# Kernel tuning notes

Measured on AMD Instinct MI355X. Metric: run time of the kernel, lower is better.

## Reference

```python
import jax, jax.numpy as jnp
import numpy as np

EMBED = 1024
DSTATE = 16
DCONV = 4
DTRANK = 64  # ceil(EMBED/16)
B = 2
T = 2048


def setup_inputs() -> dict:
    key = jax.random.key(0)
    ks = jax.random.split(key, 8)
    def w(k, shape, s=0.02):
        return jax.random.normal(k, shape, dtype=jnp.float32) * s
    return dict(
        x=jax.random.normal(ks[0], (B, T, EMBED), dtype=jnp.float32),
        in_proj_w=w(ks[1], (2 * EMBED, EMBED)), in_proj_b=jnp.zeros((2 * EMBED,), jnp.float32),
        conv_w=w(ks[2], (EMBED, 1, DCONV)), conv_b=jnp.zeros((EMBED,), jnp.float32),
        x_proj_w=w(ks[3], (DTRANK + 2 * DSTATE, EMBED)), x_proj_b=jnp.zeros((DTRANK + 2 * DSTATE,), jnp.float32),
        dt_proj_w=w(ks[4], (EMBED, DTRANK)), dt_proj_b=jnp.zeros((EMBED,), jnp.float32),
        A_log=jnp.log(jnp.arange(1, DSTATE + 1, dtype=jnp.float32))[None, :],  # (1,N) as in torch module
        D_param=jnp.ones((EMBED,), jnp.float32),
        out_proj_w=w(ks[5], (EMBED, EMBED)), out_proj_b=jnp.zeros((EMBED,), jnp.float32),
        skip_proj_w=w(ks[6], (EMBED, EMBED)), skip_proj_b=jnp.zeros((EMBED,), jnp.float32),
    )


def reference(x, in_proj_w, in_proj_b, conv_w, conv_b, x_proj_w, x_proj_b,
              dt_proj_w, dt_proj_b, A_log, D_param, out_proj_w, out_proj_b,
              skip_proj_w, skip_proj_b):
    Bsz, Tlen, Dm = x.shape
    # in_proj and split into ssm branch and gate branch
    xr = x @ in_proj_w.T + in_proj_b            # (B,T,2D)
    x_in, res = jnp.split(xr, 2, axis=-1)
    # depthwise causal conv1d (torch pads both sides then slices [:T] == left-pad)
    xc = jax.lax.conv_general_dilated(
        x_in.transpose(0, 2, 1), conv_w, (1,), [(DCONV - 1, 0)],
        dimension_numbers=('NCH', 'OIH', 'NCH'), feature_group_count=Dm)
    xc = (xc + conv_b[None, :, None]).transpose(0, 2, 1)  # (B,T,D)
    xc = jax.nn.silu(xc)
    # input-dependent SSM params
    ssm = xc @ x_proj_w.T + x_proj_b            # (B,T,dt_rank+2N)
    delta, Bp, Cp = jnp.split(ssm, [DTRANK, DTRANK + DSTATE], axis=-1)
    delta = jax.nn.softplus(delta @ dt_proj_w.T + dt_proj_b)  # (B,T,D)
    A = -jnp.exp(A_log)                          # (1,N)
    dA = jnp.exp(delta[..., None] * A)           # (B,T,D,N)
    dBu = delta[..., None] * Bp[:, :, None, :] * xc[..., None]  # (B,T,D,N)
    # inclusive associative scan over time: h_t = dA_t * h_{t-1} + dBu_t
    def op(l, r):
        Ai, Bi = l
        Aj, Bj = r
        return (Aj * Ai, Bj + Aj * Bi)
    _, ys = jax.lax.associative_scan(op, (dA, dBu), axis=1)
    y = (ys * Cp[:, :, None, :]).sum(-1)         # (B,T,D)
    y = y + xc * D_param
    y = y * jax.nn.silu(res)
    return y @ out_proj_w.T + out_proj_b + (x @ skip_proj_w.T + skip_proj_b)
```

## Files before the change

### kernel.cpp

```cpp
#include <hip/hip_runtime.h>
#include <math.h>

#define EMBED  1024
#define DSTATE 16
#define DCONV  4
#define DTRANK 64
#define BB     2
#define TT     2048
#define M_TOK  (BB*TT)
#define SSMW   96
#define NCHUNK 64
#define CLEN   (TT/NCHUNK)
#define KSPLIT 8

typedef __attribute__((ext_vector_type(8))) __bf16 bf16x8;
typedef __attribute__((ext_vector_type(4))) float floatx4;

__device__ __forceinline__ float silu_f(float x) {
    return x / (1.0f + __expf(-x));
}
__device__ __forceinline__ float softplus_f(float x) {
    return fmaxf(x, 0.0f) + log1pf(__expf(-fabsf(x)));
}
__device__ __forceinline__ unsigned short f2bf(float f) {
    union { float f; unsigned int u; } v; v.f = f;
    unsigned int u = v.u;
    return (unsigned short)((u + 0x7fffu + ((u >> 16) & 1u)) >> 16);
}
__device__ __forceinline__ float bf2f(unsigned short s) {
    union { unsigned int u; float f; } v; v.u = ((unsigned int)s) << 16;
    return v.f;
}
__device__ __forceinline__ void async16(unsigned short* lds, const unsigned short* g) {
    __builtin_amdgcn_global_load_lds(
        (const __attribute__((address_space(1))) unsigned int*)g,
        (__attribute__((address_space(3))) unsigned int*)lds, 16, 0, 0);
}

#define GEMM_DECODE \
    const int tid = threadIdx.x; const int wid = tid >> 6; \
    const int lane = tid & 63; \
    const int wm = wid >> 1, wn = wid & 1; \
    const int lr = lane & 15; const int lq = lane >> 4;

__device__ __forceinline__ void gemm_acc(
    const unsigned short* __restrict__ A, int lda,
    const unsigned short* __restrict__ W, int ldw,
    int m0, int n0, int k0, int klen, floatx4 (&acc)[4][4])
{
    __shared__ unsigned short As[128 * 32];
    __shared__ unsigned short Ws[128 * 32];
    GEMM_DECODE;
    const int l0 = tid,       row0 = l0 >> 2, kc0 = (l0 & 3) * 8;
    const int l1 = tid + 256, row1 = l1 >> 2, kc1 = (l1 & 3) * 8;

    for (int kt = k0; kt < k0 + klen; kt += 32) {
        async16(&As[l0 * 8], A + (size_t)(m0 + row0) * lda + kt + kc0);
        async16(&As[l1 * 8], A + (size_t)(m0 + row1) * lda + kt + kc1);
        async16(&Ws[l0 * 8], W + (size_t)(n0 + row0) * ldw + kt + kc0);
        async16(&Ws[l1 * 8], W + (size_t)(n0 + row1) * ldw + kt + kc1);
        __syncthreads();

        bf16x8 af[4], bfr[4];
        #pragma unroll
        for (int i = 0; i < 4; ++i)
            af[i] = *(const bf16x8*)&As[(wm * 64 + i * 16 + lr) * 32 + lq * 8];
        #pragma unroll
        for (int i = 0; i < 4; ++i)
            bfr[i] = *(const bf16x8*)&Ws[(wn * 64 + i * 16 + lr) * 32 + lq * 8];

        #pragma unroll
        for (int mi = 0; mi < 4; ++mi)
            #pragma unroll
            for (int ni = 0; ni < 4; ++ni)
                acc[mi][ni] = __builtin_amdgcn_mfma_f32_16x16x32_bf16(
                    af[mi], bfr[ni], acc[mi][ni], 0, 0, 0);
        __syncthreads();
    }
}

__global__ __launch_bounds__(256)
void gemm_in(const unsigned short* __restrict__ A,
             const unsigned short* __restrict__ W,
             const float* __restrict__ bias,
             float* __restrict__ xr, unsigned short* __restrict__ gate)
{
    floatx4 acc[4][4] = {};
    const int m0 = blockIdx.x * 128, n0 = blockIdx.y * 128;
    gemm_acc(A, 2 * EMBED, W, EMBED, m0, n0, 0, EMBED, acc);
    GEMM_DECODE;
    #pragma unroll
    for (int mi = 0; mi < 4; ++mi)
        #pragma unroll
        for (int ni = 0; ni < 4; ++ni) {
            int nb = n0 + wn * 64 + ni * 16 + lr;
            #pragma unroll
            for (int r = 0; r < 4; ++r) {
                int m = m0 + wm * 64 + mi * 16 + lq * 4 + r;
                float v = acc[mi][ni][r] + bias[nb];
                if (nb < EMBED) xr[(size_t)m * EMBED + nb] = v;
                else gate[(size_t)m * EMBED + nb - EMBED] = f2bf(silu_f(v));
            }
        }
}

__global__ __launch_bounds__(256)
void gemm_xp(const unsigned short* __restrict__ A,
             const unsigned short* __restrict__ W,
             float* __restrict__ xpart)
{
    floatx4 acc[4][4] = {};
    const int m0 = blockIdx.x * 128;
    const int k0 = blockIdx.z * (EMBED / KSPLIT);
    gemm_acc(A, EMBED, W, EMBED, m0, 0, k0, EMBED / KSPLIT, acc);
    GEMM_DECODE;
    float* base = xpart + (size_t)blockIdx.z * M_TOK * SSMW;
    #pragma unroll
    for (int mi = 0; mi < 4; ++mi)
        #pragma unroll
        for (int ni = 0; ni < 4; ++ni) {
            int nb = wn * 64 + ni * 16 + lr;
            if (nb < SSMW) {
                #pragma unroll
                for (int r = 0; r < 4; ++r) {
                    int m = m0 + wm * 64 + mi * 16 + lq * 4 + r;
                    base[(size_t)m * SSMW + nb] = acc[mi][ni][r];
                }
            }
        }
}

__global__ __launch_bounds__(256)
void xp_merge(const float* __restrict__ xpart, const float* __restrict__ xp_b,
              float* __restrict__ ssm, unsigned short* __restrict__ dtin)
{
    int idx = blockIdx.x * 256 + threadIdx.x;
    if (idx >= M_TOK * SSMW) return;
    int m = idx / SSMW, n = idx - m * SSMW;
    float s = xp_b[n];
    #pragma unroll
    for (int z = 0; z < KSPLIT; ++z) s += xpart[(size_t)z * M_TOK * SSMW + idx];
    ssm[idx] = s;
    if (n < DTRANK) dtin[(size_t)m * DTRANK + n] = f2bf(s);
}

__global__ __launch_bounds__(256)
void gemm_dt(const unsigned short* __restrict__ A,
             const unsigned short* __restrict__ W,
             const float* __restrict__ bias,
             unsigned short* __restrict__ dltb)
{
    floatx4 acc[4][4] = {};
    const int m0 = blockIdx.x * 128, n0 = blockIdx.y * 128;
    gemm_acc(A, DTRANK, W, DTRANK, m0, n0, 0, DTRANK, acc);
    GEMM_DECODE;
    #pragma unroll
    for (int mi = 0; mi < 4; ++mi)
        #pragma unroll
        for (int ni = 0; ni < 4; ++ni) {
            int nb = n0 + wn * 64 + ni * 16 + lr;
            #pragma unroll
            for (int r = 0; r < 4; ++r) {
                int m = m0 + wm * 64 + mi * 16 + lq * 4 + r;
                dltb[(size_t)m * EMBED + nb] = f2bf(softplus_f(acc[mi][ni][r] + bias[nb]));
            }
        }
}

__global__ __launch_bounds__(256)
void gemm_out(const unsigned short* __restrict__ A,
              const unsigned short* __restrict__ W,
              const float* __restrict__ bias, const float* __restrict__ bias2,
              float* __restrict__ C)
{
    floatx4 acc[4][4] = {};
    const int m0 = blockIdx.x * 128, n0 = blockIdx.y * 128;
    gemm_acc(A, 2 * EMBED, W, 2 * EMBED, m0, n0, 0, 2 * EMBED, acc);
    GEMM_DECODE;
    #pragma unroll
    for (int mi = 0; mi < 4; ++mi)
        #pragma unroll
        for (int ni = 0; ni < 4; ++ni) {
            int nb = n0 + wn * 64 + ni * 16 + lr;
            float bb = bias[nb] + bias2[nb];
            #pragma unroll
            for (int r = 0; r < 4; ++r) {
                int m = m0 + wm * 64 + mi * 16 + lq * 4 + r;
                C[(size_t)m * EMBED + nb] = acc[mi][ni][r] + bb;
            }
        }
}

#define SEG0 524288
#define SEG1 (SEG0 + 16384)
#define SEG2 (SEG1 + 32768)
#define SEG3 (SEG2 + 524288)
#define SEG4 (SEG3 + 1048576)

__global__ __launch_bounds__(256)
void cvt_pack(const float* __restrict__ in_w, const float* __restrict__ dt_w,
              const float* __restrict__ xp_w, const float* __restrict__ ow,
              const float* __restrict__ sw, const float* __restrict__ x,
              unsigned short* __restrict__ inwb, unsigned short* __restrict__ dtwb,
              unsigned short* __restrict__ xpwb, unsigned short* __restrict__ wcat,
              unsigned short* __restrict__ Acat)
{
    int j = blockIdx.x * 256 + threadIdx.x;
    if (j >= SEG4) return;
    float4 v = {0.f, 0.f, 0.f, 0.f};
    unsigned short* dst;
    if (j < SEG0) {
        v = *(const float4*)&in_w[j * 4];
        dst = &inwb[j * 4];
    } else if (j < SEG1) {
        int i = (j - SEG0) * 4;
        v = *(const float4*)&dt_w[i];
        dst = &dtwb[i];
    } else if (j < SEG2) {
        int i = (j - SEG1) * 4;
        if ((i >> 10) < SSMW) v = *(const float4*)&xp_w[i];
        dst = &xpwb[i];
    } else if (j < SEG3) {
        int i = (j - SEG2) * 4;
        int n = i >> 11, k = i & 2047;
        v = *(const float4*)((k < EMBED) ? &ow[(size_t)n * EMBED + k]
                                         : &sw[(size_t)n * EMBED + (k - EMBED)]);
        dst = &wcat[i];
    } else {
        int i = (j - SEG3) * 4;
        int m = i >> 10, k = i & 1023;
        v = *(const float4*)&x[i];
        dst = &Acat[(size_t)m * 2 * EMBED + EMBED + k];
    }
    ushort4 o = { f2bf(v.x), f2bf(v.y), f2bf(v.z), f2bf(v.w) };
    *(ushort4*)dst = o;
}

__global__ __launch_bounds__(256)
void conv_silu(const float* __restrict__ xr,
               const float* __restrict__ conv_w,
               const float* __restrict__ conv_b,
               unsigned short* __restrict__ xcb)
{
    int idx = blockIdx.x * 256 + threadIdx.x;
    if (idx >= BB * TT * EMBED / 4) return;
    int dq = idx & (EMBED / 4 - 1);
    int t  = (idx >> 8) & (TT - 1);
    int b  = idx >> 19;
    int d  = dq * 4;

    float4 cw0 = *(const float4*)&conv_w[(d + 0) * 4];
    float4 cw1 = *(const float4*)&conv_w[(d + 1) * 4];
    float4 cw2 = *(const float4*)&conv_w[(d + 2) * 4];
    float4 cw3 = *(const float4*)&conv_w[(d + 3) * 4];
    float4 s   = *(const float4*)&conv_b[d];

    const float* w0 = (const float*)&cw0;
    const float* w1 = (const float*)&cw1;
    const float* w2 = (const float*)&cw2;
    const float* w3 = (const float*)&cw3;

    #pragma unroll
    for (int jj = 0; jj < 4; ++jj) {
        int tr = t - 3 + jj;
        if (tr >= 0) {
            float4 v = *(const float4*)&xr[(size_t)(b * TT + tr) * EMBED + d];
            s.x = fmaf(w0[jj], v.x, s.x);
            s.y = fmaf(w1[jj], v.y, s.y);
            s.z = fmaf(w2[jj], v.z, s.z);
            s.w = fmaf(w3[jj], v.w, s.w);
        }
    }
    ushort4 o = { f2bf(silu_f(s.x)), f2bf(silu_f(s.y)),
                  f2bf(silu_f(s.z)), f2bf(silu_f(s.w)) };
    *(ushort4*)&xcb[(size_t)(b * TT + t) * EMBED + d] = o;
}

__global__ __launch_bounds__(256)
void scan_chunk(const unsigned short* __restrict__ deltab,
                const unsigned short* __restrict__ xcb,
                const float* __restrict__ ssm,
                const float* __restrict__ A_log,
                float* __restrict__ hout,
                float* __restrict__ Ssum)
{
    __shared__ float Bs[CLEN][DSTATE];
    const int tid = threadIdx.x;
    const int blk = blockIdx.x;
    const int dg = blk & 3, chunk = (blk >> 2) & (NCHUNK - 1), b = blk >> 8;
    const int d = dg * 256 + tid;
    const int t0 = chunk * CLEN;

    for (int i = tid; i < CLEN * DSTATE; i += 256) {
        int t = i >> 4, n = i & 15;
        Bs[t][n] = ssm[(size_t)(b * TT + t0 + t) * SSMW + DTRANK + n];
    }
    __syncthreads();

    float An[DSTATE];
    #pragma unroll
    for (int n = 0; n < DSTATE; ++n) An[n] = -__expf(A_log[n]);

    float h[DSTATE] = {};
    float S = 0.f;
    for (int t = 0; t < CLEN; ++t) {
        size_t row = (size_t)(b * TT + t0 + t);
        float dv = bf2f(deltab[row * EMBED + d]);
        float xv = bf2f(xcb[row * EMBED + d]);
        S += dv;
        float sx = dv * xv;
        float Bv[DSTATE];
        *(float4*)&Bv[0]  = *(const float4*)&Bs[t][0];
        *(float4*)&Bv[4]  = *(const float4*)&Bs[t][4];
        *(float4*)&Bv[8]  = *(const float4*)&Bs[t][8];
        *(float4*)&Bv[12] = *(const float4*)&Bs[t][12];
        #pragma unroll
        for (int n = 0; n < DSTATE; ++n) {
            float dA = __expf(dv * An[n]);
            h[n] = fmaf(dA, h[n], sx * Bv[n]);
        }
    }
    size_t base = ((size_t)(chunk * BB + b) * EMBED + d) * DSTATE;
    #pragma unroll
    for (int jj = 0; jj < 4; ++jj)
        *(float4*)&hout[base + jj * 4] = *(float4*)&h[jj * 4];
    Ssum[(size_t)(chunk * BB + b) * EMBED + d] = S;
}

__global__ __launch_bounds__(256)
void scan_combine(const float* __restrict__ A_log,
                  const float* __restrict__ Ssum,
                  const float* __restrict__ hout,
                  float* __restrict__ hin)
{
    int idx = blockIdx.x * 256 + threadIdx.x;
    int n  = idx & 15;
    int bd = idx >> 4;
    float An = -__expf(A_log[n]);
    float h = 0.f;
    for (int c0 = 0; c0 < NCHUNK; c0 += 8) {
        float ho[8], S[8];
        #pragma unroll
        for (int jj = 0; jj < 8; ++jj) {
            ho[jj] = hout[(size_t)(c0 + jj) * (BB * EMBED * DSTATE) + idx];
            S[jj]  = Ssum[(size_t)(c0 + jj) * (BB * EMBED) + bd];
        }
        #pragma unroll
        for (int jj = 0; jj < 8; ++jj) {
            hin[(size_t)(c0 + jj) * (BB * EMBED * DSTATE) + idx] = h;
            h = fmaf(__expf(An * S[jj]), h, ho[jj]);
        }
    }
}

__global__ __launch_bounds__(256)
void scan_apply(const unsigned short* __restrict__ deltab,
                const unsigned short* __restrict__ xcb,
                const float* __restrict__ ssm,
                const float* __restrict__ A_log,
                const float* __restrict__ D_param,
                const unsigned short* __restrict__ gate,
                const float* __restrict__ hin,
                unsigned short* __restrict__ Acat)
{
    __shared__ float Bs[CLEN][DSTATE];
    __shared__ float Cs[CLEN][DSTATE];
    const int tid = threadIdx.x;
    const int blk = blockIdx.x;
    const int dg = blk & 3, chunk = (blk >> 2) & (NCHUNK - 1), b = blk >> 8;
    const int d = dg * 256 + tid;
    const int t0 = chunk * CLEN;

    for (int i = tid; i < CLEN * DSTATE; i += 256) {
        int t = i >> 4, n = i & 15;
        size_t row = (size_t)(b * TT + t0 + t);
        Bs[t][n] = ssm[row * SSMW + DTRANK + n];
        Cs[t][n] = ssm[row * SSMW + DTRANK + DSTATE + n];
    }
    __syncthreads();

    float An[DSTATE];
    #pragma unroll
    for (int n = 0; n < DSTATE; ++n) An[n] = -__expf(A_log[n]);
    float Dd = D_param[d];

    float h[DSTATE];
    size_t base = ((size_t)(chunk * BB + b) * EMBED + d) * DSTATE;
    #pragma unroll
    for (int jj = 0; jj < 4; ++jj)
        *(float4*)&h[jj * 4] = *(const float4*)&hin[base + jj * 4];

    for (int t = 0; t < CLEN; ++t) {
        size_t row = (size_t)(b * TT + t0 + t);
        float dv = bf2f(deltab[row * EMBED + d]);
        float xv = bf2f(xcb[row * EMBED + d]);
        float sx = dv * xv;
        float Bv[DSTATE], Cv[DSTATE];
        *(float4*)&Bv[0]  = *(const float4*)&Bs[t][0];
        *(float4*)&Bv[4]  = *(const float4*)&Bs[t][4];
        *(float4*)&Bv[8]  = *(const float4*)&Bs[t][8];
        *(float4*)&Bv[12] = *(const float4*)&Bs[t][12];
        *(float4*)&Cv[0]  = *(const float4*)&Cs[t][0];
        *(float4*)&Cv[4]  = *(const float4*)&Cs[t][4];
        *(float4*)&Cv[8]  = *(const float4*)&Cs[t][8];
        *(float4*)&Cv[12] = *(const float4*)&Cs[t][12];
        float y0 = 0.f, y1 = 0.f, y2 = 0.f, y3 = 0.f;
        #pragma unroll
        for (int n = 0; n < DSTATE; n += 4) {
            float dA0 = __expf(dv * An[n + 0]);
            float dA1 = __expf(dv * An[n + 1]);
            float dA2 = __expf(dv * An[n + 2]);
            float dA3 = __expf(dv * An[n + 3]);
            h[n + 0] = fmaf(dA0, h[n + 0], sx * Bv[n + 0]);
            h[n + 1] = fmaf(dA1, h[n + 1], sx * Bv[n + 1]);
            h[n + 2] = fmaf(dA2, h[n + 2], sx * Bv[n + 2]);
            h[n + 3] = fmaf(dA3, h[n + 3], sx * Bv[n + 3]);
            y0 = fmaf(h[n + 0], Cv[n + 0], y0);
            y1 = fmaf(h[n + 1], Cv[n + 1], y1);
            y2 = fmaf(h[n + 2], Cv[n + 2], y2);
            y3 = fmaf(h[n + 3], Cv[n + 3], y3);
        }
        float yv = (y0 + y1) + (y2 + y3) + xv * Dd;
        float g = bf2f(gate[row * EMBED + d]);
        Acat[row * 2 * EMBED + d] = f2bf(yv * g);
    }
}

extern "C" void kernel_launch(void* const* d_in, const int* in_sizes, int n_in,
                              void* d_out, int out_size, void* d_ws, size_t ws_size,
                              hipStream_t stream) {
    const float* x      = (const float*)d_in[0];
    const float* in_w   = (const float*)d_in[1];
    const float* in_b   = (const float*)d_in[2];
    const float* conv_w = (const float*)d_in[3];
    const float* conv_b = (const float*)d_in[4];
    const float* xp_w   = (const float*)d_in[5];
    const float* xp_b   = (const float*)d_in[6];
    const float* dt_w   = (const float*)d_in[7];
    const float* dt_b   = (const float*)d_in[8];
    const float* A_log  = (const float*)d_in[9];
    const float* Dp     = (const float*)d_in[10];
    const float* out_w  = (const float*)d_in[11];
    const float* out_b  = (const float*)d_in[12];
    const float* skip_w = (const float*)d_in[13];
    const float* skip_b = (const float*)d_in[14];
    float* out = (float*)d_out;

    float* ws    = (float*)d_ws;
    float* xr    = ws;
    float* ssm   = xr    + (size_t)M_TOK * EMBED;
    float* xpart = ssm   + (size_t)M_TOK * SSMW;
    float* hout  = xpart + (size_t)KSPLIT * M_TOK * SSMW;
    float* hin   = hout  + (size_t)NCHUNK * BB * EMBED * DSTATE;
    float* Ssum  = hin   + (size_t)NCHUNK * BB * EMBED * DSTATE;
    unsigned short* Acat = (unsigned short*)(Ssum + (size_t)NCHUNK * BB * EMBED);
    unsigned short* xcb  = Acat + (size_t)M_TOK * 2 * EMBED;
    unsigned short* dltb = xcb  + (size_t)M_TOK * EMBED;
    unsigned short* dtin = dltb + (size_t)M_TOK * EMBED;
    unsigned short* gate = dtin + (size_t)M_TOK * DTRANK;
    unsigned short* inwb = gate + (size_t)M_TOK * EMBED;
    unsigned short* xpwb = inwb + (size_t)2 * EMBED * EMBED;
    unsigned short* dtwb = xpwb + (size_t)128 * EMBED;
    unsigned short* wcat = dtwb + (size_t)EMBED * DTRANK;

    dim3 blk(256);

    cvt_pack<<<(SEG4 + 255) / 256, blk, 0, stream>>>(
        in_w, dt_w, xp_w, out_w, skip_w, x, inwb, dtwb, xpwb, wcat, Acat);

    gemm_in<<<dim3(M_TOK / 128, 2 * EMBED / 128), blk, 0, stream>>>(
        Acat + EMBED, inwb, in_b, xr, gate);

    conv_silu<<<(M_TOK * EMBED / 4 + 255) / 256, blk, 0, stream>>>(
        xr, conv_w, conv_b, xcb);

    gemm_xp<<<dim3(M_TOK / 128, 1, KSPLIT), blk, 0, stream>>>(xcb, xpwb, xpart);
    xp_merge<<<(M_TOK * SSMW + 255) / 256, blk, 0, stream>>>(xpart, xp_b, ssm, dtin);

    gemm_dt<<<dim3(M_TOK / 128, EMBED / 128), blk, 0, stream>>>(
        dtin, dtwb, dt_b, dltb);

    scan_chunk<<<BB * NCHUNK * (EMBED / 256), blk, 0, stream>>>(
        dltb, xcb, ssm, A_log, hout, Ssum);
    scan_combine<<<(BB * EMBED * DSTATE + 255) / 256, blk, 0, stream>>>(
        A_log, Ssum, hout, hin);
    scan_apply<<<BB * NCHUNK * (EMBED / 256), blk, 0, stream>>>(
        dltb, xcb, ssm, A_log, Dp, gate, hin, Acat);

    gemm_out<<<dim3(M_TOK / 128, EMBED / 128), blk, 0, stream>>>(
        Acat, wcat, out_b, skip_b, out);
}
```

Baseline: 278.9 us.

## Deepen GEMM K-tile to 64, store xr in bf16, split-K gemm_out with atomics

The shared GEMM loop now stages 64-wide K tiles instead of 32, which halves the number of barrier pairs per K and doubles the MFMA work done per sync. The in_proj SSM branch is written as bf16 instead of fp32, cutting the write and the later conv read traffic. gemm_out is split 4 ways over K with float atomicAdd into an output zeroed beforehand, giving 256→1024 blocks for better CU occupancy. The cost is an extra zeroing kernel, atomic traffic, nondeterministic summation order, and a small precision loss in the conv input.

```diff
diff --git a/kernel.cpp b/kernel.cpp
--- a/kernel.cpp
+++ b/kernel.cpp
@@ -48,33 +48,42 @@
     const unsigned short* __restrict__ W, int ldw,
     int m0, int n0, int k0, int klen, floatx4 (&acc)[4][4])
 {
-    __shared__ unsigned short As[128 * 32];
-    __shared__ unsigned short Ws[128 * 32];
+    __shared__ unsigned short As[128 * 64];
+    __shared__ unsigned short Ws[128 * 64];
     GEMM_DECODE;
-    const int l0 = tid,       row0 = l0 >> 2, kc0 = (l0 & 3) * 8;
-    const int l1 = tid + 256, row1 = l1 >> 2, kc1 = (l1 & 3) * 8;
-
-    for (int kt = k0; kt < k0 + klen; kt += 32) {
-        async16(&As[l0 * 8], A + (size_t)(m0 + row0) * lda + kt + kc0);
-        async16(&As[l1 * 8], A + (size_t)(m0 + row1) * lda + kt + kc1);
-        async16(&Ws[l0 * 8], W + (size_t)(n0 + row0) * ldw + kt + kc0);
-        async16(&Ws[l1 * 8], W + (size_t)(n0 + row1) * ldw + kt + kc1);
+
+    for (int kt = k0; kt < k0 + klen; kt += 64) {
+        #pragma unroll
+        for (int j = 0; j < 4; ++j) {
+            int idx = tid + j * 256;
+            int row = idx >> 3, kc = (idx & 7) * 8;
+            async16(&As[idx * 8], A + (size_t)(m0 + row) * lda + kt + kc);
+        }
+        #pragma unroll
+        for (int j = 0; j < 4; ++j) {
+            int idx = tid + j * 256;
+            int row = idx >> 3, kc = (idx & 7) * 8;
+            async16(&Ws[idx * 8], W + (size_t)(n0 + row) * ldw + kt + kc);
+        }
         __syncthreads();
 
-        bf16x8 af[4], bfr[4];
-        #pragma unroll
-        for (int i = 0; i < 4; ++i)
-            af[i] = *(const bf16x8*)&As[(wm * 64 + i * 16 + lr) * 32 + lq * 8];
-        #pragma unroll
-        for (int i = 0; i < 4; ++i)
-            bfr[i] = *(const bf16x8*)&Ws[(wn * 64 + i * 16 + lr) * 32 + lq * 8];
-
-        #pragma unroll
-        for (int mi = 0; mi < 4; ++mi)
+        #pragma unroll
+        for (int ks = 0; ks < 64; ks += 32) {
+            bf16x8 af[4], bfr[4];
             #pragma unroll
-            for (int ni = 0; ni < 4; ++ni)
-                acc[mi][ni] = __builtin_amdgcn_mfma_f32_16x16x32_bf16(
-                    af[mi], bfr[ni], acc[mi][ni], 0, 0, 0);
+            for (int i = 0; i < 4; ++i)
+                af[i] = *(const bf16x8*)&As[(wm * 64 + i * 16 + lr) * 64 + ks + lq * 8];
+            #pragma unroll
+            for (int i = 0; i < 4; ++i)
+                bfr[i] = *(const bf16x8*)&Ws[(wn * 64 + i * 16 + lr) * 64 + ks + lq * 8];
+
+            #pragma unroll
+            for (int mi = 0; mi < 4; ++mi)
+                #pragma unroll
+                for (int ni = 0; ni < 4; ++ni)
+                    acc[mi][ni] = __builtin_amdgcn_mfma_f32_16x16x32_bf16(
+                        af[mi], bfr[ni], acc[mi][ni], 0, 0, 0);
+        }
         __syncthreads();
     }
 }
@@ -83,7 +92,7 @@
 void gemm_in(const unsigned short* __restrict__ A,
              const unsigned short* __restrict__ W,
              const float* __restrict__ bias,
-             float* __restrict__ xr, unsigned short* __restrict__ gate)
+             unsigned short* __restrict__ xrb, unsigned short* __restrict__ gate)
 {
     floatx4 acc[4][4] = {};
     const int m0 = blockIdx.x * 128, n0 = blockIdx.y * 128;
@@ -98,7 +107,7 @@
             for (int r = 0; r < 4; ++r) {
                 int m = m0 + wm * 64 + mi * 16 + lq * 4 + r;
                 float v = acc[mi][ni][r] + bias[nb];
-                if (nb < EMBED) xr[(size_t)m * EMBED + nb] = v;
+                if (nb < EMBED) xrb[(size_t)m * EMBED + nb] = f2bf(v);
                 else gate[(size_t)m * EMBED + nb - EMBED] = f2bf(silu_f(v));
             }
         }
@@ -168,6 +177,16 @@
 }
 
 __global__ __launch_bounds__(256)
+void zero_out(float* __restrict__ C)
+{
+    int i = (blockIdx.x * 256 + threadIdx.x) * 4;
+    if (i < M_TOK * EMBED) {
+        float4 z = {0.f, 0.f, 0.f, 0.f};
+        *(float4*)&C[i] = z;
+    }
+}
+
+__global__ __launch_bounds__(256)
 void gemm_out(const unsigned short* __restrict__ A,
               const unsigned short* __restrict__ W,
               const float* __restrict__ bias, const float* __restrict__ bias2,
@@ -175,18 +194,20 @@
 {
     floatx4 acc[4][4] = {};
     const int m0 = blockIdx.x * 128, n0 = blockIdx.y * 128;
-    gemm_acc(A, 2 * EMBED, W, 2 * EMBED, m0, n0, 0, 2 * EMBED, acc);
+    const int k0 = blockIdx.z * 512;
+    gemm_acc(A, 2 * EMBED, W, 2 * EMBED, m0, n0, k0, 512, acc);
     GEMM_DECODE;
+    const bool addb = (blockIdx.z == 0);
     #pragma unroll
     for (int mi = 0; mi < 4; ++mi)
         #pragma unroll
         for (int ni = 0; ni < 4; ++ni) {
             int nb = n0 + wn * 64 + ni * 16 + lr;
-            float bb = bias[nb] + bias2[nb];
+            float bb = addb ? (bias[nb] + bias2[nb]) : 0.f;
             #pragma unroll
             for (int r = 0; r < 4; ++r) {
                 int m = m0 + wm * 64 + mi * 16 + lq * 4 + r;
-                C[(size_t)m * EMBED + nb] = acc[mi][ni][r] + bb;
+                atomicAdd(&C[(size_t)m * EMBED + nb], acc[mi][ni][r] + bb);
             }
         }
 }
@@ -237,7 +258,7 @@
 }
 
 __global__ __launch_bounds__(256)
-void conv_silu(const float* __restrict__ xr,
+void conv_silu(const unsigned short* __restrict__ xrb,
                const float* __restrict__ conv_w,
                const float* __restrict__ conv_b,
                unsigned short* __restrict__ xcb)
@@ -264,11 +285,11 @@
     for (int jj = 0; jj < 4; ++jj) {
         int tr = t - 3 + jj;
         if (tr >= 0) {
-            float4 v = *(const float4*)&xr[(size_t)(b * TT + tr) * EMBED + d];
-            s.x = fmaf(w0[jj], v.x, s.x);
-            s.y = fmaf(w1[jj], v.y, s.y);
-            s.z = fmaf(w2[jj], v.z, s.z);
-            s.w = fmaf(w3[jj], v.w, s.w);
+            ushort4 u = *(const ushort4*)&xrb[(size_t)(b * TT + tr) * EMBED + d];
+            s.x = fmaf(w0[jj], bf2f(u.x), s.x);
+            s.y = fmaf(w1[jj], bf2f(u.y), s.y);
+            s.z = fmaf(w2[jj], bf2f(u.z), s.z);
+            s.w = fmaf(w3[jj], bf2f(u.w), s.w);
         }
     }
     ushort4 o = { f2bf(silu_f(s.x)), f2bf(silu_f(s.y)),
@@ -447,14 +468,14 @@
     float* out = (float*)d_out;
 
     float* ws    = (float*)d_ws;
-    float* xr    = ws;
-    float* ssm   = xr    + (size_t)M_TOK * EMBED;
+    float* ssm   = ws;
     float* xpart = ssm   + (size_t)M_TOK * SSMW;
     float* hout  = xpart + (size_t)KSPLIT * M_TOK * SSMW;
     float* hin   = hout  + (size_t)NCHUNK * BB * EMBED * DSTATE;
     float* Ssum  = hin   + (size_t)NCHUNK * BB * EMBED * DSTATE;
     unsigned short* Acat = (unsigned short*)(Ssum + (size_t)NCHUNK * BB * EMBED);
-    unsigned short* xcb  = Acat + (size_t)M_TOK * 2 * EMBED;
+    unsigned short* xrb  = Acat + (size_t)M_TOK * 2 * EMBED;
+    unsigned short* xcb  = xrb  + (size_t)M_TOK * EMBED;
     unsigned short* dltb = xcb  + (size_t)M_TOK * EMBED;
     unsigned short* dtin = dltb + (size_t)M_TOK * EMBED;
     unsigned short* gate = dtin + (size_t)M_TOK * DTRANK;
@@ -467,12 +488,13 @@
 
     cvt_pack<<<(SEG4 + 255) / 256, blk, 0, stream>>>(
         in_w, dt_w, xp_w, out_w, skip_w, x, inwb, dtwb, xpwb, wcat, Acat);
+    zero_out<<<(M_TOK * EMBED / 4 + 255) / 256, blk, 0, stream>>>(out);
 
     gemm_in<<<dim3(M_TOK / 128, 2 * EMBED / 128), blk, 0, stream>>>(
-        Acat + EMBED, inwb, in_b, xr, gate);
+        Acat + EMBED, inwb, in_b, xrb, gate);
 
     conv_silu<<<(M_TOK * EMBED / 4 + 255) / 256, blk, 0, stream>>>(
-        xr, conv_w, conv_b, xcb);
+        xrb, conv_w, conv_b, xcb);
 
     gemm_xp<<<dim3(M_TOK / 128, 1, KSPLIT), blk, 0, stream>>>(xcb, xpwb, xpart);
     xp_merge<<<(M_TOK * SSMW + 255) / 256, blk, 0, stream>>>(xpart, xp_b, ssm, dtin);
@@ -487,6 +509,6 @@
     scan_apply<<<BB * NCHUNK * (EMBED / 256), blk, 0, stream>>>(
         dltb, xcb, ssm, A_log, Dp, gate, hin, Acat);
 
-    gemm_out<<<dim3(M_TOK / 128, EMBED / 128), blk, 0, stream>>>(
+    gemm_out<<<dim3(M_TOK / 128, EMBED / 128, 4), blk, 0, stream>>>(
         Acat, wcat, out_b, skip_b, out);
 }
```

After: 370.8 us. 32.9% more time.
